# Kernel optimization log

Hardware: AMD Instinct MI355X
Metric: run time of the kernel (lower is better)

Reference implementation:

```python
import jax, jax.numpy as jnp
import numpy as np

NC = 4
X = Y = Z = 64
IMG_SHAPE = (96, 96, 96)
SPAN = 2          # FILTER_SIZE = [5,5,5]
NUM_ITER = 4
DIL = 2           # DILATION = 2.0
SMOOTH_DISTANCE_INIT = 0.3
PRIOR_DISTANCE_INIT = 0.3


def _ind(d):
    # mirrors _get_ind from the torch code
    return (d, 0) if d > 0 else (0, -d)


def _sl(a, b):
    # slice(a, -b) with -0 -> None, mirrors _negative
    return slice(a, -b if b else None)


def _offsets():
    for dx in range(-SPAN, SPAN + 1):
        for dy in range(-SPAN, SPAN + 1):
            for dz in range(-SPAN, SPAN + 1):
                yield dx, dy, dz


def _lin_resize_axis(x, axis, out):
    # 1D linear interpolation matching torch align_corners=True
    n = x.shape[axis]
    if out == n:
        return x
    pos = jnp.arange(out, dtype=x.dtype) * ((n - 1) / (out - 1))
    i0 = jnp.clip(jnp.floor(pos).astype(jnp.int32), 0, n - 1)
    i1 = jnp.clip(i0 + 1, 0, n - 1)
    w = pos - i0.astype(x.dtype)
    shp = [1] * x.ndim
    shp[axis] = out
    w = w.reshape(shp)
    return jnp.take(x, i0, axis=axis) * (1 - w) + jnp.take(x, i1, axis=axis) * w


def _resize3d(x, out_sz):
    # trilinear, align_corners=True, separable over the 3 spatial axes of [b,c,X,Y,Z]
    for ax, o in zip((2, 3, 4), out_sz):
        x = _lin_resize_axis(x, ax, o)
    return x


def _smooth_gaussian(feats):
    # feats: [b, c, X, Y, Z] -> gaussian [b, 5,5,5, X, Y, Z]
    b = feats.shape[0]
    sp = feats.shape[2:]
    g = jnp.zeros((b, 5, 5, 5) + sp, feats.dtype)
    for dx, dy, dz in _offsets():
        dx1, dx2 = _ind(dx); dy1, dy2 = _ind(dy); dz1, dz2 = _ind(dz)
        a = feats[:, :, _sl(dx1, dx2), _sl(dy1, dy2), _sl(dz1, dz2)]
        c = feats[:, :, _sl(dx2, dx1), _sl(dy2, dy1), _sl(dz2, dz1)]
        e = jnp.exp(-0.5 * jnp.sum((a - c) ** 2, axis=1))
        g = g.at[:, dx + SPAN, dy + SPAN, dz + SPAN,
                 _sl(dx2, dx1), _sl(dy2, dy1), _sl(dz2, dz1)].set(e)
    return g


def _prior_gaussian(f1, f2):
    # f1, f2: [b, c, x, y, z] (already downsampled) -> [b, 5,5,5, x, y, z]
    b = f1.shape[0]
    sp = f1.shape[2:]
    g = jnp.zeros((b, 5, 5, 5) + sp, f1.dtype)
    for dx, dy, dz in _offsets():
        dx1, dx2 = _ind(dx); dy1, dy2 = _ind(dy); dz1, dz2 = _ind(dz)
        a = f1[:, :, _sl(dx2, dx1), _sl(dy2, dy1), _sl(dz2, dz1)]
        c = f2[:, :, _sl(dx1, dx2), _sl(dy1, dy2), _sl(dz1, dz2)]
        e = jnp.exp(-0.5 * jnp.sum((a - c) ** 2, axis=1))
        g = g.at[:, dx + SPAN, dy + SPAN, dz + SPAN,
                 _sl(dx2, dx1), _sl(dy2, dy1), _sl(dz2, dz1)].set(e)
    return g


def _message(p, g):
    # p: [b, nc, x, y, z]; g: [b, 5,5,5, x, y, z]
    out = jnp.zeros_like(p)
    for dx, dy, dz in _offsets():
        dx1, dx2 = _ind(dx); dy1, dy2 = _ind(dy); dz1, dz2 = _ind(dz)
        a = p[:, :, _sl(dx1, dx2), _sl(dy1, dy2), _sl(dz1, dz2)]
        w = g[:, None, dx + SPAN, dy + SPAN, dz + SPAN,
              _sl(dx2, dx1), _sl(dy2, dy1), _sl(dz2, dz1)]
        out = out.at[:, :, _sl(dx2, dx1), _sl(dy2, dy1), _sl(dz2, dz1)].add(a * w)
    return out


def setup_inputs() -> dict:
    key = jax.random.key(0)
    ks = jax.random.split(key, 6)
    unary = jax.random.normal(ks[0], (1, NC, X, Y, Z), jnp.float32)
    img = jax.random.normal(ks[1], (1, 2, X, Y, Z), jnp.float32)
    atlas = jax.random.normal(ks[2], (1, 2, X, Y, Z), jnp.float32)
    atlas_label = jax.random.uniform(ks[3], (1, X, Y, Z, NC), jnp.float32)
    patch_start = jax.random.randint(ks[4], (1, 3), 0, 32, jnp.int32)
    return {
        "unary": unary,
        "img": img,
        "atlas": atlas,
        "atlas_label": atlas_label,
        "patch_start": patch_start,
        "smooth_norm": jnp.array([1.0 / SMOOTH_DISTANCE_INIT], jnp.float32),
        "smooth_weight": jnp.ones((NC,), jnp.float32),
        "prior_norm": jnp.array([1.0 / PRIOR_DISTANCE_INIT], jnp.float32),
        "prior_weight": jnp.ones(IMG_SHAPE, jnp.float32),
        "compat_w": jnp.eye(NC, dtype=jnp.float32),
    }


def reference(unary, img, atlas, atlas_label, patch_start,
              smooth_norm, smooth_weight, prior_norm, prior_weight, compat_w):
    b, nc, x, y, z = unary.shape
    ds = (x // DIL, y // DIL, z // DIL)  # floor(in*0.5) == ceil(in/2) for even dims

    # similarity kernels
    sg = _smooth_gaussian(img * smooth_norm)                      # [b,5,5,5,x,y,z]
    f1 = _resize3d(img * prior_norm, ds)
    f2 = _resize3d(atlas * prior_norm, ds)
    pg = _prior_gaussian(f1, f2)                                  # [b,5,5,5,x/2,y/2,z/2]

    # prior message is independent of q_values: compute once
    al = jnp.transpose(atlas_label, (0, 4, 1, 2, 3))              # [b,nc,x,y,z]
    al_ds = _resize3d(al, ds)
    pm = _resize3d(_message(al_ds, pg), (x, y, z))                # [b,nc,x,y,z]
    pw = jax.lax.dynamic_slice(
        prior_weight,
        (patch_start[0, 0], patch_start[0, 1], patch_start[0, 2]),
        (x, y, z))
    prior_term = pw[None, None] * pm

    q = unary
    for _ in range(NUM_ITER):
        p = jax.nn.softmax(q, axis=1)
        sm = _message(p, sg)
        pred = smooth_weight[None, :, None, None, None] * sm + prior_term
        q = unary + jnp.einsum('oc,bcxyz->boxyz', compat_w, pred)  # 1x1x1 compat conv
    return q
```

## Files before the change

### kernel.cpp

```cpp
#include <hip/hip_runtime.h>

#define NN 64
#define N3 (64*64*64)
#define DS 32

#define LOG2E 1.4426950408889634f
#define FSCALE 0.8493218002880191f

typedef _Float16 h2  __attribute__((ext_vector_type(2)));
typedef __fp16   h2f __attribute__((ext_vector_type(2)));

__device__ __forceinline__ float fexp2(float x) { return __builtin_amdgcn_exp2f(x); }

__device__ __forceinline__ h2 u2h(unsigned u) { union { unsigned u; h2 h; } c; c.u = u; return c.h; }
__device__ __forceinline__ unsigned h2u(h2 h) { union { unsigned u; h2 h; } c; c.h = h; return c.u; }
__device__ __forceinline__ h2 pkh(float a, float b) {
    union { h2f a; h2 b; } c; c.a = __builtin_amdgcn_cvt_pkrtz(a, b); return c.b;
}
__device__ __forceinline__ float fdot2(h2 a, h2 b) {
    union { h2 h; h2f f; } ca, cb; ca.h = a; cb.h = b;
    return __builtin_amdgcn_fdot2(ca.f, cb.f, 0.0f, false);
}


#define TXD 8
#define TYD 8
#define TZD 8
#define TZR 4
#define RZ 2
#define HX 12
#define HY 12
#define HZ 12
#define PZ 14
#define CPX 6
#define CSX 10

template<bool FIRST, bool LAST>
__global__ __launch_bounds__(1024, 8) void k_iter(
    const float* __restrict__ unary,
    const uint2* __restrict__ pin,
    const unsigned* __restrict__ fpk_in,
    const float* __restrict__ img,
    const float* __restrict__ atlas,
    const float* __restrict__ alabel,
    const float* __restrict__ pnorm,
    const float* __restrict__ snorm,
    const float* __restrict__ pweight,
    const int* __restrict__ pstart,
    const float* __restrict__ sweight,
    const float* __restrict__ compat,
    float4* __restrict__ unary4,
    unsigned* __restrict__ fpk_out,
    uint2* __restrict__ pout,
    float* __restrict__ qout)
{
    __shared__ __align__(16) unsigned char raw1[16384];
    auto nbS = reinterpret_cast<uint4 (*)[CSX][CSX]>(raw1);
    auto pS  = reinterpret_cast<uint2 (*)[HY][PZ]>(raw1);
    __shared__ __align__(8)  unsigned fS[HX][HY][PZ];
    __shared__ __align__(16) uint4    accS[3][TXD*TYD*TZR];
    __shared__ __align__(8)  uint2    pmS[CPX][CPX][CPX];

    const int tzg = threadIdx.x, ty = threadIdx.y;
    const int tx = threadIdx.z & 7, s = threadIdx.z >> 3;
    const int x0b = blockIdx.z * TXD, y0b = blockIdx.y * TYD, z0b = blockIdx.x * TZD;
    const int tid = threadIdx.x + TZR*threadIdx.y + (TZR*TYD)*threadIdx.z;

    const int tz0 = tzg * RZ;
    const int gx = x0b + tx, gy = y0b + ty;
    const int g = (gx*NN + gy)*NN + z0b + tz0;

    float4 u40, u41;
    float sw0, sw1, sw2, sw3;
    float cw[16];

    if (FIRST) {
        const int cxlo = (x0b*31)/63, cylo = (y0b*31)/63, czlo = (z0b*31)/63;
        const float pnf = pnorm[0] * FSCALE;

        if (tid < CSX*CSX*CSX) {
            int lz = tid % CSX; int r = tid / CSX; int ly = r % CSX; int lx = r / CSX;
            int cx = cxlo - 2 + lx, cy = cylo - 2 + ly, cz = czlo - 2 + lz;
            uint4 v = make_uint4(0u, 0u, 0u, 0u);
            if ((unsigned)cx < DS && (unsigned)cy < DS && (unsigned)cz < DS) {
                const float scale = 63.0f / 31.0f;
                float posx = cx*scale; int a0i = (int)posx; float wx = posx - a0i; int a1i = a0i+1 <= 63 ? a0i+1 : 63;
                float posy = cy*scale; int b0i = (int)posy; float wy = posy - b0i; int b1i = b0i+1 <= 63 ? b0i+1 : 63;
                float posz = cz*scale; int d0i = (int)posz; float wz = posz - d0i; int d1i = d0i+1 <= 63 ? d0i+1 : 63;
                float w000=(1-wx)*(1-wy)*(1-wz), w001=(1-wx)*(1-wy)*wz;
                float w010=(1-wx)*wy*(1-wz),     w011=(1-wx)*wy*wz;
                float w100=wx*(1-wy)*(1-wz),     w101=wx*(1-wy)*wz;
                float w110=wx*wy*(1-wz),         w111=wx*wy*wz;
                int c000=(a0i*NN+b0i)*NN+d0i, c001=(a0i*NN+b0i)*NN+d1i;
                int c010=(a0i*NN+b1i)*NN+d0i, c011=(a0i*NN+b1i)*NN+d1i;
                int c100=(a1i*NN+b0i)*NN+d0i, c101=(a1i*NN+b0i)*NN+d1i;
                int c110=(a1i*NN+b1i)*NN+d0i, c111=(a1i*NN+b1i)*NN+d1i;
                auto tri = [&](const float* p) -> float {
                    return p[c000]*w000 + p[c001]*w001 + p[c010]*w010 + p[c011]*w011
                         + p[c100]*w100 + p[c101]*w101 + p[c110]*w110 + p[c111]*w111;
                };
                const float4* lab = (const float4*)alabel;
                float4 l = make_float4(0.f,0.f,0.f,0.f);
                {
                    float4 t;
                    t = lab[c000]; l.x += w000*t.x; l.y += w000*t.y; l.z += w000*t.z; l.w += w000*t.w;
                    t = lab[c001]; l.x += w001*t.x; l.y += w001*t.y; l.z += w001*t.z; l.w += w001*t.w;
                    t = lab[c010]; l.x += w010*t.x; l.y += w010*t.y; l.z += w010*t.z; l.w += w010*t.w;
                    t = lab[c011]; l.x += w011*t.x; l.y += w011*t.y; l.z += w011*t.z; l.w += w011*t.w;
                    t = lab[c100]; l.x += w100*t.x; l.y += w100*t.y; l.z += w100*t.z; l.w += w100*t.w;
                    t = lab[c101]; l.x += w101*t.x; l.y += w101*t.y; l.z += w101*t.z; l.w += w101*t.w;
                    t = lab[c110]; l.x += w110*t.x; l.y += w110*t.y; l.z += w110*t.z; l.w += w110*t.w;
                    t = lab[c111]; l.x += w111*t.x; l.y += w111*t.y; l.z += w111*t.z; l.w += w111*t.w;
                }
                v = make_uint4(h2u(pkh(pnf*tri(atlas), pnf*tri(atlas + N3))),
                               h2u(pkh(l.x, l.y)), h2u(pkh(l.z, l.w)),
                               h2u(pkh(pnf*tri(img), pnf*tri(img + N3))));
            }
            nbS[lx][ly][lz] = v;
        }
        __syncthreads();

        if (tid < CPX*CPX*CPX) {
            int pz = tid % CPX; int r = tid / CPX; int py = r % CPX; int px = r / CPX;
            int cx = cxlo + px, cy = cylo + py, cz = czlo + pz;
            uint2 o = make_uint2(0u, 0u);
            if (cx < DS && cy < DS && cz < DS) {
                h2 ncf = -u2h(nbS[px+2][py+2][pz+2].w);
                float a0=0.f, a1=0.f, a2=0.f, a3=0.f;
                for (int dx = -2; dx <= 2; ++dx) {
                    int xx = cx + dx; if ((unsigned)xx >= DS) continue;
                    for (int dy = -2; dy <= 2; ++dy) {
                        int yy = cy + dy; if ((unsigned)yy >= DS) continue;
                        #pragma unroll
                        for (int dz = -2; dz <= 2; ++dz) {
                            int zz = cz + dz; if ((unsigned)zz >= DS) continue;
                            uint4 v = nbS[px+2+dx][py+2+dy][pz+2+dz];
                            h2 d = u2h(v.x) + ncf;
                            float w = fexp2(-fdot2(d, d));
                            h2 l01 = u2h(v.y), l23 = u2h(v.z);
                            a0 += w*(float)l01.x; a1 += w*(float)l01.y;
                            a2 += w*(float)l23.x; a3 += w*(float)l23.y;
                        }
                    }
                }
                o = make_uint2(h2u(pkh(a0, a1)), h2u(pkh(a2, a3)));
            }
            pmS[px][py][pz] = o;
        }
        __syncthreads();

        if (s == 0) {
            sw0 = sweight[0]; sw1 = sweight[1]; sw2 = sweight[2]; sw3 = sweight[3];
            #pragma unroll
            for (int k = 0; k < 16; ++k) cw[k] = compat[k];

            const float S13 = 31.0f / 63.0f;
            float posx = gx*S13; int xc0 = (int)posx; float wxf = posx - xc0; int xc1 = xc0 < 31 ? xc0+1 : 31;
            float posy = gy*S13; int yc0 = (int)posy; float wyf = posy - yc0; int yc1 = yc0 < 31 ? yc0+1 : 31;
            int lx0 = xc0-cxlo, lx1 = xc1-cxlo;
            int ly0 = yc0-cylo, ly1 = yc1-cylo;
            const int ps0 = pstart[0], ps1 = pstart[1], ps2 = pstart[2];

            auto up = [&](uint2 u) -> float4 {
                h2 a = u2h(u.x), b = u2h(u.y);
                return make_float4((float)a.x, (float)a.y, (float)b.x, (float)b.y);
            };

            #pragma unroll
            for (int rz = 0; rz < RZ; ++rz) {
                int gz = z0b + tz0 + rz;
                float posz = gz*S13; int zc0 = (int)posz; float wzf = posz - zc0; int zc1 = zc0 < 31 ? zc0+1 : 31;
                int lz0 = zc0-czlo, lz1 = zc1-czlo;
                float4 p000 = up(pmS[lx0][ly0][lz0]), p001 = up(pmS[lx0][ly0][lz1]);
                float4 p010 = up(pmS[lx0][ly1][lz0]), p011 = up(pmS[lx0][ly1][lz1]);
                float4 p100 = up(pmS[lx1][ly0][lz0]), p101 = up(pmS[lx1][ly0][lz1]);
                float4 p110 = up(pmS[lx1][ly1][lz0]), p111 = up(pmS[lx1][ly1][lz1]);
                float w000=(1-wxf)*(1-wyf)*(1-wzf), w001=(1-wxf)*(1-wyf)*wzf;
                float w010=(1-wxf)*wyf*(1-wzf),     w011=(1-wxf)*wyf*wzf;
                float w100=wxf*(1-wyf)*(1-wzf),     w101=wxf*(1-wyf)*wzf;
                float w110=wxf*wyf*(1-wzf),         w111=wxf*wyf*wzf;
                float pw = pweight[(ps0+gx)*96*96 + (ps1+gy)*96 + (ps2+gz)];
                float pr0 = pw*(w000*p000.x + w001*p001.x + w010*p010.x + w011*p011.x + w100*p100.x + w101*p101.x + w110*p110.x + w111*p111.x);
                float pr1 = pw*(w000*p000.y + w001*p001.y + w010*p010.y + w011*p011.y + w100*p100.y + w101*p101.y + w110*p110.y + w111*p111.y);
                float pr2 = pw*(w000*p000.z + w001*p001.z + w010*p010.z + w011*p011.z + w100*p100.z + w101*p101.z + w110*p110.z + w111*p111.z);
                float pr3 = pw*(w000*p000.w + w001*p001.w + w010*p010.w + w011*p011.w + w100*p100.w + w101*p101.w + w110*p110.w + w111*p111.w);

                int gg = g + rz;
                float4 q;
                q.x = unary[gg]      + cw[0]*pr0  + cw[1]*pr1  + cw[2]*pr2  + cw[3]*pr3;
                q.y = unary[gg+N3]   + cw[4]*pr0  + cw[5]*pr1  + cw[6]*pr2  + cw[7]*pr3;
                q.z = unary[gg+2*N3] + cw[8]*pr0  + cw[9]*pr1  + cw[10]*pr2 + cw[11]*pr3;
                q.w = unary[gg+3*N3] + cw[12]*pr0 + cw[13]*pr1 + cw[14]*pr2 + cw[15]*pr3;
                unary4[gg] = q;
                if (rz == 0) u40 = q; else u41 = q;
            }
        }
        __syncthreads();
    }

    const float sc = FIRST ? snorm[0] * FSCALE : 0.0f;
    #pragma unroll
    for (int rr = 0; rr < 2; ++rr) {
        int i = tid + rr*1024;
        if (i < HX*HY*HZ) {
            int lz = i % HZ; int r = i / HZ;
            int ly = r % HY; int lx = r / HY;
            int hgx = x0b + lx - 2, hgy = y0b + ly - 2, hgz = z0b + lz - 2;
            uint2 pu = make_uint2(0u, 0u);
            unsigned fu = 0u;
            if ((unsigned)hgx < NN && (unsigned)hgy < NN && (unsigned)hgz < NN) {
                int hg = (hgx*NN + hgy)*NN + hgz;
                if (FIRST) {
                    float q0 = unary[hg], q1 = unary[hg+N3], q2 = unary[hg+2*N3], q3 = unary[hg+3*N3];
                    float m = fmaxf(fmaxf(q0,q1), fmaxf(q2,q3));
                    float e0 = fexp2((q0-m)*LOG2E);
                    float e1 = fexp2((q1-m)*LOG2E);
                    float e2 = fexp2((q2-m)*LOG2E);
                    float e3 = fexp2((q3-m)*LOG2E);
                    float inv = 1.0f/(e0+e1+e2+e3);
                    pu = make_uint2(h2u(pkh(e0*inv, e1*inv)), h2u(pkh(e2*inv, e3*inv)));
                    fu = h2u(pkh(img[hg]*sc, img[hg+N3]*sc));
                    if ((unsigned)(lx-2) < 8u && (unsigned)(ly-2) < 8u && (unsigned)(lz-2) < 8u)
                        fpk_out[hg] = fu;
                } else {
                    pu = pin[hg];
                    fu = fpk_in[hg];
                }
            }
            pS[lx][ly][lz] = pu;
            fS[lx][ly][lz] = fu;
        }
    }

    if (!FIRST && s == 0) {
        u40 = unary4[g]; u41 = unary4[g+1];
        sw0 = sweight[0]; sw1 = sweight[1]; sw2 = sweight[2]; sw3 = sweight[3];
        #pragma unroll
        for (int k = 0; k < 16; ++k) cw[k] = compat[k];
    }

    __syncthreads();

    const h2 ncf0 = -u2h(fS[tx+2][ty+2][tz0+2]);
    const h2 ncf1 = -u2h(fS[tx+2][ty+2][tz0+3]);

    h2 a01_0 = (h2)0, a23_0 = (h2)0, a01_1 = (h2)0, a23_1 = (h2)0;

    #pragma unroll
    for (int pp = 0; pp < 7; ++pp) {
        int p = (3 - s) + 4*pp;
        if (p < 25) {
            int dx = p / 5, dy = p - 5*dx;
            const uint4* pv = reinterpret_cast<const uint4*>(&pS[tx+dx][ty+dy][tz0]);
            const uint2* fv = reinterpret_cast<const uint2*>(&fS[tx+dx][ty+dy][tz0]);
            uint4 qa = pv[0], qb = pv[1], qc = pv[2];
            uint2 fa = fv[0], fb = fv[1], fc = fv[2];

            unsigned fz[6]  = { fa.x, fa.y, fb.x, fb.y, fc.x, fc.y };
            unsigned p01[6] = { qa.x, qa.z, qb.x, qb.z, qc.x, qc.z };
            unsigned p23[6] = { qa.y, qa.w, qb.y, qb.w, qc.y, qc.w };

            #pragma unroll
            for (int dz = 0; dz < 5; ++dz) {
                {
                    h2 d = u2h(fz[dz]) + ncf0;
                    float w = fexp2(-fdot2(d, d));
                    h2 w2 = pkh(w, w);
                    a01_0 = w2 * u2h(p01[dz]) + a01_0;
                    a23_0 = w2 * u2h(p23[dz]) + a23_0;
                }
                {
                    h2 d = u2h(fz[dz+1]) + ncf1;
                    float w = fexp2(-fdot2(d, d));
                    h2 w2 = pkh(w, w);
                    a01_1 = w2 * u2h(p01[dz+1]) + a01_1;
                    a23_1 = w2 * u2h(p23[dz+1]) + a23_1;
                }
            }
        }
    }

    const int pid = (tx*TYD + ty)*TZR + tzg;
    if (s != 0) {
        accS[s-1][pid] = make_uint4(h2u(a01_0), h2u(a23_0), h2u(a01_1), h2u(a23_1));
    }
    __syncthreads();

    if (s == 0) {
        #pragma unroll
        for (int j = 0; j < 3; ++j) {
            uint4 v = accS[j][pid];
            a01_0 += u2h(v.x); a23_0 += u2h(v.y);
            a01_1 += u2h(v.z); a23_1 += u2h(v.w);
        }

        float p0, p1, p2, p3;
        float r00, r10, r20, r30, r01, r11, r21, r31;
        p0 = sw0*(float)a01_0.x; p1 = sw1*(float)a01_0.y;
        p2 = sw2*(float)a23_0.x; p3 = sw3*(float)a23_0.y;
        r00 = u40.x + cw[0]*p0  + cw[1]*p1  + cw[2]*p2  + cw[3]*p3;
        r10 = u40.y + cw[4]*p0  + cw[5]*p1  + cw[6]*p2  + cw[7]*p3;
        r20 = u40.z + cw[8]*p0  + cw[9]*p1  + cw[10]*p2 + cw[11]*p3;
        r30 = u40.w + cw[12]*p0 + cw[13]*p1 + cw[14]*p2 + cw[15]*p3;
        p0 = sw0*(float)a01_1.x; p1 = sw1*(float)a01_1.y;
        p2 = sw2*(float)a23_1.x; p3 = sw3*(float)a23_1.y;
        r01 = u41.x + cw[0]*p0  + cw[1]*p1  + cw[2]*p2  + cw[3]*p3;
        r11 = u41.y + cw[4]*p0  + cw[5]*p1  + cw[6]*p2  + cw[7]*p3;
        r21 = u41.z + cw[8]*p0  + cw[9]*p1  + cw[10]*p2 + cw[11]*p3;
        r31 = u41.w + cw[12]*p0 + cw[13]*p1 + cw[14]*p2 + cw[15]*p3;

        if (LAST) {
            *(float2*)(qout + 0*N3 + g) = make_float2(r00, r01);
            *(float2*)(qout + 1*N3 + g) = make_float2(r10, r11);
            *(float2*)(qout + 2*N3 + g) = make_float2(r20, r21);
            *(float2*)(qout + 3*N3 + g) = make_float2(r30, r31);
        } else {
            float m0 = fmaxf(fmaxf(r00,r10), fmaxf(r20,r30));
            float e00 = fexp2((r00-m0)*LOG2E), e10 = fexp2((r10-m0)*LOG2E);
            float e20 = fexp2((r20-m0)*LOG2E), e30 = fexp2((r30-m0)*LOG2E);
            float i0 = 1.0f/(e00+e10+e20+e30);
            float m1 = fmaxf(fmaxf(r01,r11), fmaxf(r21,r31));
            float e01 = fexp2((r01-m1)*LOG2E), e11 = fexp2((r11-m1)*LOG2E);
            float e21 = fexp2((r21-m1)*LOG2E), e31 = fexp2((r31-m1)*LOG2E);
            float i1 = 1.0f/(e01+e11+e21+e31);
            uint4 o = make_uint4(h2u(pkh(e00*i0, e10*i0)), h2u(pkh(e20*i0, e30*i0)),
                                 h2u(pkh(e01*i1, e11*i1)), h2u(pkh(e21*i1, e31*i1)));
            *reinterpret_cast<uint4*>(&pout[g]) = o;
        }
    }
}


extern "C" void kernel_launch(void* const* d_in, const int* in_sizes, int n_in,
                              void* d_out, int out_size, void* d_ws, size_t ws_size,
                              hipStream_t stream)
{
    const float* unary   = (const float*)d_in[0];
    const float* img     = (const float*)d_in[1];
    const float* atlas   = (const float*)d_in[2];
    const float* alabel  = (const float*)d_in[3];
    const int*   pstart  = (const int*)d_in[4];
    const float* snorm   = (const float*)d_in[5];
    const float* sweight = (const float*)d_in[6];
    const float* pnorm   = (const float*)d_in[7];
    const float* pweight = (const float*)d_in[8];
    const float* compat  = (const float*)d_in[9];
    float* out = (float*)d_out;
    float* ws  = (float*)d_ws;

    float4*   unary4 = (float4*)ws;
    uint2*    pA     = (uint2*)(ws + 4*N3);
    uint2*    pB     = (uint2*)(ws + 6*N3);
    unsigned* fpk    = (unsigned*)(ws + 8*N3);

    dim3 grid(NN/TZD, NN/TYD, NN/TXD), block(TZR, TYD, 32);
    k_iter<true, false><<<grid, block, 0, stream>>>(unary, pA, fpk, img, atlas, alabel,
        pnorm, snorm, pweight, pstart, sweight, compat, unary4, fpk, pA, out);
    k_iter<false,false><<<grid, block, 0, stream>>>(unary, pA, fpk, img, atlas, alabel,
        pnorm, snorm, pweight, pstart, sweight, compat, unary4, fpk, pB, out);
    k_iter<false,false><<<grid, block, 0, stream>>>(unary, pB, fpk, img, atlas, alabel,
        pnorm, snorm, pweight, pstart, sweight, compat, unary4, fpk, pA, out);
    k_iter<false,true ><<<grid, block, 0, stream>>>(unary, pA, fpk, img, atlas, alabel,
        pnorm, snorm, pweight, pstart, sweight, compat, unary4, fpk, pB, out);
}
```

Baseline: 90.90 us.

## Fuse pairs of mean-field iterations per launch via halo recompute

Replaces four per-iteration kernel launches with two fused launches, each running two iterations. The intermediate softmax is recomputed on a widened 12^3 halo region in shared memory, so one global round trip of the probability field and one launch boundary are removed per pair. The packed feature array is no longer written and read back from global memory; it is rebuilt from the image in each kernel. In exchange there is redundant halo computation, a larger shared-memory footprint that may cut occupancy, and more per-block work in the first stage.

```diff
diff --git a/kernel.cpp b/kernel.cpp
--- a/kernel.cpp
+++ b/kernel.cpp
@@ -23,23 +23,18 @@
 }
 
 
-#define TXD 8
-#define TYD 8
-#define TZD 8
-#define TZR 4
-#define RZ 2
-#define HX 12
-#define HY 12
-#define HZ 12
-#define PZ 14
-#define CPX 6
-#define CSX 10
-
-template<bool FIRST, bool LAST>
-__global__ __launch_bounds__(1024, 8) void k_iter(
+#define TB 8
+#define HE 16
+#define PZ2 18
+#define DE 12
+#define PZ1 14
+#define CPX 8
+#define CSX 12
+
+template<bool FIRST>
+__global__ __launch_bounds__(1024, 8) void k_fused(
     const float* __restrict__ unary,
     const uint2* __restrict__ pin,
-    const unsigned* __restrict__ fpk_in,
     const float* __restrict__ img,
     const float* __restrict__ atlas,
     const float* __restrict__ alabel,
@@ -50,78 +45,94 @@
     const float* __restrict__ sweight,
     const float* __restrict__ compat,
     float4* __restrict__ unary4,
-    unsigned* __restrict__ fpk_out,
     uint2* __restrict__ pout,
     float* __restrict__ qout)
 {
-    __shared__ __align__(16) unsigned char raw1[16384];
-    auto nbS = reinterpret_cast<uint4 (*)[CSX][CSX]>(raw1);
-    auto pS  = reinterpret_cast<uint2 (*)[HY][PZ]>(raw1);
-    __shared__ __align__(8)  unsigned fS[HX][HY][PZ];
-    __shared__ __align__(16) uint4    accS[3][TXD*TYD*TZR];
-    __shared__ __align__(8)  uint2    pmS[CPX][CPX][CPX];
-
-    const int tzg = threadIdx.x, ty = threadIdx.y;
-    const int tx = threadIdx.z & 7, s = threadIdx.z >> 3;
-    const int x0b = blockIdx.z * TXD, y0b = blockIdx.y * TYD, z0b = blockIdx.x * TZD;
-    const int tid = threadIdx.x + TZR*threadIdx.y + (TZR*TYD)*threadIdx.z;
-
-    const int tz0 = tzg * RZ;
-    const int gx = x0b + tx, gy = y0b + ty;
-    const int g = (gx*NN + gy)*NN + z0b + tz0;
-
-    float4 u40, u41;
-    float sw0, sw1, sw2, sw3;
+    __shared__ __align__(16) unsigned char region1[HE*HE*PZ2*8];
+    __shared__ __align__(16) unsigned char region2[12288];
+    __shared__ __align__(8)  unsigned fS[HE][HE][PZ2];
+
+    auto p2S  = reinterpret_cast<uint2 (*)[HE][PZ2]>(region1);
+    auto p1S  = reinterpret_cast<uint2 (*)[DE][PZ1]>(region1);
+    auto nbS  = reinterpret_cast<uint4 (*)[CSX][CSX]>(region1);
+    auto pmS  = reinterpret_cast<uint2 (*)[CPX][CPX]>(region2);
+    auto accS = reinterpret_cast<uint4 (*)[256]>(region2);
+
+    const int tid = threadIdx.x;
+    const int x0b = blockIdx.z * TB, y0b = blockIdx.y * TB, z0b = blockIdx.x * TB;
+    const float sc = snorm[0] * FSCALE;
+
+    const float sw0 = sweight[0], sw1 = sweight[1], sw2 = sweight[2], sw3 = sweight[3];
     float cw[16];
+    #pragma unroll
+    for (int k = 0; k < 16; ++k) cw[k] = compat[k];
+
+    const bool mact = tid < 864;
+    const int  mpz = tid % 6;
+    const int  mt  = tid / 6;
+    const int  mpy = mt % 12;
+    const int  mpx = mt / 12;
+    const int  mlz0 = 2 * mpz;
+    const int  mgx = x0b - 2 + mpx, mgy = y0b - 2 + mpy, mgz0 = z0b - 2 + mlz0;
+
+    float4 mu4[2];
+    mu4[0] = make_float4(0.f,0.f,0.f,0.f);
+    mu4[1] = make_float4(0.f,0.f,0.f,0.f);
 
     if (FIRST) {
-        const int cxlo = (x0b*31)/63, cylo = (y0b*31)/63, czlo = (z0b*31)/63;
+        const int cxlo = (((x0b-2 > 0) ? x0b-2 : 0) * 31) / 63;
+        const int cylo = (((y0b-2 > 0) ? y0b-2 : 0) * 31) / 63;
+        const int czlo = (((z0b-2 > 0) ? z0b-2 : 0) * 31) / 63;
         const float pnf = pnorm[0] * FSCALE;
 
-        if (tid < CSX*CSX*CSX) {
-            int lz = tid % CSX; int r = tid / CSX; int ly = r % CSX; int lx = r / CSX;
-            int cx = cxlo - 2 + lx, cy = cylo - 2 + ly, cz = czlo - 2 + lz;
-            uint4 v = make_uint4(0u, 0u, 0u, 0u);
-            if ((unsigned)cx < DS && (unsigned)cy < DS && (unsigned)cz < DS) {
-                const float scale = 63.0f / 31.0f;
-                float posx = cx*scale; int a0i = (int)posx; float wx = posx - a0i; int a1i = a0i+1 <= 63 ? a0i+1 : 63;
-                float posy = cy*scale; int b0i = (int)posy; float wy = posy - b0i; int b1i = b0i+1 <= 63 ? b0i+1 : 63;
-                float posz = cz*scale; int d0i = (int)posz; float wz = posz - d0i; int d1i = d0i+1 <= 63 ? d0i+1 : 63;
-                float w000=(1-wx)*(1-wy)*(1-wz), w001=(1-wx)*(1-wy)*wz;
-                float w010=(1-wx)*wy*(1-wz),     w011=(1-wx)*wy*wz;
-                float w100=wx*(1-wy)*(1-wz),     w101=wx*(1-wy)*wz;
-                float w110=wx*wy*(1-wz),         w111=wx*wy*wz;
-                int c000=(a0i*NN+b0i)*NN+d0i, c001=(a0i*NN+b0i)*NN+d1i;
-                int c010=(a0i*NN+b1i)*NN+d0i, c011=(a0i*NN+b1i)*NN+d1i;
-                int c100=(a1i*NN+b0i)*NN+d0i, c101=(a1i*NN+b0i)*NN+d1i;
-                int c110=(a1i*NN+b1i)*NN+d0i, c111=(a1i*NN+b1i)*NN+d1i;
-                auto tri = [&](const float* p) -> float {
-                    return p[c000]*w000 + p[c001]*w001 + p[c010]*w010 + p[c011]*w011
-                         + p[c100]*w100 + p[c101]*w101 + p[c110]*w110 + p[c111]*w111;
-                };
-                const float4* lab = (const float4*)alabel;
-                float4 l = make_float4(0.f,0.f,0.f,0.f);
-                {
-                    float4 t;
-                    t = lab[c000]; l.x += w000*t.x; l.y += w000*t.y; l.z += w000*t.z; l.w += w000*t.w;
-                    t = lab[c001]; l.x += w001*t.x; l.y += w001*t.y; l.z += w001*t.z; l.w += w001*t.w;
-                    t = lab[c010]; l.x += w010*t.x; l.y += w010*t.y; l.z += w010*t.z; l.w += w010*t.w;
-                    t = lab[c011]; l.x += w011*t.x; l.y += w011*t.y; l.z += w011*t.z; l.w += w011*t.w;
-                    t = lab[c100]; l.x += w100*t.x; l.y += w100*t.y; l.z += w100*t.z; l.w += w100*t.w;
-                    t = lab[c101]; l.x += w101*t.x; l.y += w101*t.y; l.z += w101*t.z; l.w += w101*t.w;
-                    t = lab[c110]; l.x += w110*t.x; l.y += w110*t.y; l.z += w110*t.z; l.w += w110*t.w;
-                    t = lab[c111]; l.x += w111*t.x; l.y += w111*t.y; l.z += w111*t.z; l.w += w111*t.w;
-                }
-                v = make_uint4(h2u(pkh(pnf*tri(atlas), pnf*tri(atlas + N3))),
-                               h2u(pkh(l.x, l.y)), h2u(pkh(l.z, l.w)),
-                               h2u(pkh(pnf*tri(img), pnf*tri(img + N3))));
-            }
-            nbS[lx][ly][lz] = v;
+        #pragma unroll
+        for (int r = 0; r < 2; ++r) {
+            int i = tid + r*1024;
+            if (i < CSX*CSX*CSX) {
+                int lz = i % CSX; int t = i / CSX; int ly = t % CSX; int lx = t / CSX;
+                int cx = cxlo - 2 + lx, cy = cylo - 2 + ly, cz = czlo - 2 + lz;
+                uint4 v = make_uint4(0u, 0u, 0u, 0u);
+                if ((unsigned)cx < DS && (unsigned)cy < DS && (unsigned)cz < DS) {
+                    const float scale = 63.0f / 31.0f;
+                    float posx = cx*scale; int a0i = (int)posx; float wx = posx - a0i; int a1i = a0i+1 <= 63 ? a0i+1 : 63;
+                    float posy = cy*scale; int b0i = (int)posy; float wy = posy - b0i; int b1i = b0i+1 <= 63 ? b0i+1 : 63;
+                    float posz = cz*scale; int d0i = (int)posz; float wz = posz - d0i; int d1i = d0i+1 <= 63 ? d0i+1 : 63;
+                    float w000=(1-wx)*(1-wy)*(1-wz), w001=(1-wx)*(1-wy)*wz;
+                    float w010=(1-wx)*wy*(1-wz),     w011=(1-wx)*wy*wz;
+                    float w100=wx*(1-wy)*(1-wz),     w101=wx*(1-wy)*wz;
+                    float w110=wx*wy*(1-wz),         w111=wx*wy*wz;
+                    int c000=(a0i*NN+b0i)*NN+d0i, c001=(a0i*NN+b0i)*NN+d1i;
+                    int c010=(a0i*NN+b1i)*NN+d0i, c011=(a0i*NN+b1i)*NN+d1i;
+                    int c100=(a1i*NN+b0i)*NN+d0i, c101=(a1i*NN+b0i)*NN+d1i;
+                    int c110=(a1i*NN+b1i)*NN+d0i, c111=(a1i*NN+b1i)*NN+d1i;
+                    auto tri = [&](const float* p) -> float {
+                        return p[c000]*w000 + p[c001]*w001 + p[c010]*w010 + p[c011]*w011
+                             + p[c100]*w100 + p[c101]*w101 + p[c110]*w110 + p[c111]*w111;
+                    };
+                    const float4* lab = (const float4*)alabel;
+                    float4 l = make_float4(0.f,0.f,0.f,0.f);
+                    {
+                        float4 t4;
+                        t4 = lab[c000]; l.x += w000*t4.x; l.y += w000*t4.y; l.z += w000*t4.z; l.w += w000*t4.w;
+                        t4 = lab[c001]; l.x += w001*t4.x; l.y += w001*t4.y; l.z += w001*t4.z; l.w += w001*t4.w;
+                        t4 = lab[c010]; l.x += w010*t4.x; l.y += w010*t4.y; l.z += w010*t4.z; l.w += w010*t4.w;
+                        t4 = lab[c011]; l.x += w011*t4.x; l.y += w011*t4.y; l.z += w011*t4.z; l.w += w011*t4.w;
+                        t4 = lab[c100]; l.x += w100*t4.x; l.y += w100*t4.y; l.z += w100*t4.z; l.w += w100*t4.w;
+                        t4 = lab[c101]; l.x += w101*t4.x; l.y += w101*t4.y; l.z += w101*t4.z; l.w += w101*t4.w;
+                        t4 = lab[c110]; l.x += w110*t4.x; l.y += w110*t4.y; l.z += w110*t4.z; l.w += w110*t4.w;
+                        t4 = lab[c111]; l.x += w111*t4.x; l.y += w111*t4.y; l.z += w111*t4.z; l.w += w111*t4.w;
+                    }
+                    v = make_uint4(h2u(pkh(pnf*tri(atlas), pnf*tri(atlas + N3))),
+                                   h2u(pkh(l.x, l.y)), h2u(pkh(l.z, l.w)),
+                                   h2u(pkh(pnf*tri(img), pnf*tri(img + N3))));
+                }
+                nbS[lx][ly][lz] = v;
+            }
         }
         __syncthreads();
 
         if (tid < CPX*CPX*CPX) {
-            int pz = tid % CPX; int r = tid / CPX; int py = r % CPX; int px = r / CPX;
+            int pz = tid & 7; int py = (tid >> 3) & 7; int px = tid >> 6;
             int cx = cxlo + px, cy = cylo + py, cz = czlo + pz;
             uint2 o = make_uint2(0u, 0u);
             if (cx < DS && cy < DS && cz < DS) {
@@ -149,100 +160,171 @@
         }
         __syncthreads();
 
-        if (s == 0) {
-            sw0 = sweight[0]; sw1 = sweight[1]; sw2 = sweight[2]; sw3 = sweight[3];
-            #pragma unroll
-            for (int k = 0; k < 16; ++k) cw[k] = compat[k];
-
+        if (mact) {
             const float S13 = 31.0f / 63.0f;
-            float posx = gx*S13; int xc0 = (int)posx; float wxf = posx - xc0; int xc1 = xc0 < 31 ? xc0+1 : 31;
-            float posy = gy*S13; int yc0 = (int)posy; float wyf = posy - yc0; int yc1 = yc0 < 31 ? yc0+1 : 31;
-            int lx0 = xc0-cxlo, lx1 = xc1-cxlo;
-            int ly0 = yc0-cylo, ly1 = yc1-cylo;
             const int ps0 = pstart[0], ps1 = pstart[1], ps2 = pstart[2];
-
-            auto up = [&](uint2 u) -> float4 {
-                h2 a = u2h(u.x), b = u2h(u.y);
-                return make_float4((float)a.x, (float)a.y, (float)b.x, (float)b.y);
-            };
-
-            #pragma unroll
-            for (int rz = 0; rz < RZ; ++rz) {
-                int gz = z0b + tz0 + rz;
-                float posz = gz*S13; int zc0 = (int)posz; float wzf = posz - zc0; int zc1 = zc0 < 31 ? zc0+1 : 31;
-                int lz0 = zc0-czlo, lz1 = zc1-czlo;
-                float4 p000 = up(pmS[lx0][ly0][lz0]), p001 = up(pmS[lx0][ly0][lz1]);
-                float4 p010 = up(pmS[lx0][ly1][lz0]), p011 = up(pmS[lx0][ly1][lz1]);
-                float4 p100 = up(pmS[lx1][ly0][lz0]), p101 = up(pmS[lx1][ly0][lz1]);
-                float4 p110 = up(pmS[lx1][ly1][lz0]), p111 = up(pmS[lx1][ly1][lz1]);
-                float w000=(1-wxf)*(1-wyf)*(1-wzf), w001=(1-wxf)*(1-wyf)*wzf;
-                float w010=(1-wxf)*wyf*(1-wzf),     w011=(1-wxf)*wyf*wzf;
-                float w100=wxf*(1-wyf)*(1-wzf),     w101=wxf*(1-wyf)*wzf;
-                float w110=wxf*wyf*(1-wzf),         w111=wxf*wyf*wzf;
-                float pw = pweight[(ps0+gx)*96*96 + (ps1+gy)*96 + (ps2+gz)];
-                float pr0 = pw*(w000*p000.x + w001*p001.x + w010*p010.x + w011*p011.x + w100*p100.x + w101*p101.x + w110*p110.x + w111*p111.x);
-                float pr1 = pw*(w000*p000.y + w001*p001.y + w010*p010.y + w011*p011.y + w100*p100.y + w101*p101.y + w110*p110.y + w111*p111.y);
-                float pr2 = pw*(w000*p000.z + w001*p001.z + w010*p010.z + w011*p011.z + w100*p100.z + w101*p101.z + w110*p110.z + w111*p111.z);
-                float pr3 = pw*(w000*p000.w + w001*p001.w + w010*p010.w + w011*p011.w + w100*p100.w + w101*p101.w + w110*p110.w + w111*p111.w);
-
-                int gg = g + rz;
-                float4 q;
-                q.x = unary[gg]      + cw[0]*pr0  + cw[1]*pr1  + cw[2]*pr2  + cw[3]*pr3;
-                q.y = unary[gg+N3]   + cw[4]*pr0  + cw[5]*pr1  + cw[6]*pr2  + cw[7]*pr3;
-                q.z = unary[gg+2*N3] + cw[8]*pr0  + cw[9]*pr1  + cw[10]*pr2 + cw[11]*pr3;
-                q.w = unary[gg+3*N3] + cw[12]*pr0 + cw[13]*pr1 + cw[14]*pr2 + cw[15]*pr3;
-                unary4[gg] = q;
-                if (rz == 0) u40 = q; else u41 = q;
-            }
-        }
-        __syncthreads();
-    }
-
-    const float sc = FIRST ? snorm[0] * FSCALE : 0.0f;
+            if ((unsigned)mgx < NN && (unsigned)mgy < NN) {
+                float posx = mgx*S13; int xc0 = (int)posx; float wxf = posx - xc0; int xc1 = xc0 < 31 ? xc0+1 : 31;
+                float posy = mgy*S13; int yc0 = (int)posy; float wyf = posy - yc0; int yc1 = yc0 < 31 ? yc0+1 : 31;
+                int lx0 = xc0-cxlo, lx1 = xc1-cxlo;
+                int ly0 = yc0-cylo, ly1 = yc1-cylo;
+                auto up = [&](uint2 u) -> float4 {
+                    h2 a = u2h(u.x), b = u2h(u.y);
+                    return make_float4((float)a.x, (float)a.y, (float)b.x, (float)b.y);
+                };
+                #pragma unroll
+                for (int rz = 0; rz < 2; ++rz) {
+                    int gz = mgz0 + rz;
+                    if ((unsigned)gz >= NN) continue;
+                    float posz = gz*S13; int zc0 = (int)posz; float wzf = posz - zc0; int zc1 = zc0 < 31 ? zc0+1 : 31;
+                    int lz0c = zc0-czlo, lz1c = zc1-czlo;
+                    float4 p000 = up(pmS[lx0][ly0][lz0c]), p001 = up(pmS[lx0][ly0][lz1c]);
+                    float4 p010 = up(pmS[lx0][ly1][lz0c]), p011 = up(pmS[lx0][ly1][lz1c]);
+                    float4 p100 = up(pmS[lx1][ly0][lz0c]), p101 = up(pmS[lx1][ly0][lz1c]);
+                    float4 p110 = up(pmS[lx1][ly1][lz0c]), p111 = up(pmS[lx1][ly1][lz1c]);
+                    float w000=(1-wxf)*(1-wyf)*(1-wzf), w001=(1-wxf)*(1-wyf)*wzf;
+                    float w010=(1-wxf)*wyf*(1-wzf),     w011=(1-wxf)*wyf*wzf;
+                    float w100=wxf*(1-wyf)*(1-wzf),     w101=wxf*(1-wyf)*wzf;
+                    float w110=wxf*wyf*(1-wzf),         w111=wxf*wyf*wzf;
+                    float pw = pweight[(ps0+mgx)*96*96 + (ps1+mgy)*96 + (ps2+gz)];
+                    float pr0 = pw*(w000*p000.x + w001*p001.x + w010*p010.x + w011*p011.x + w100*p100.x + w101*p101.x + w110*p110.x + w111*p111.x);
+                    float pr1 = pw*(w000*p000.y + w001*p001.y + w010*p010.y + w011*p011.y + w100*p100.y + w101*p101.y + w110*p110.y + w111*p111.y);
+                    float pr2 = pw*(w000*p000.z + w001*p001.z + w010*p010.z + w011*p011.z + w100*p100.z + w101*p101.z + w110*p110.z + w111*p111.z);
+                    float pr3 = pw*(w000*p000.w + w001*p001.w + w010*p010.w + w011*p011.w + w100*p100.w + w101*p101.w + w110*p110.w + w111*p111.w);
+                    int gg = (mgx*NN + mgy)*NN + gz;
+                    float4 q;
+                    q.x = unary[gg]      + cw[0]*pr0  + cw[1]*pr1  + cw[2]*pr2  + cw[3]*pr3;
+                    q.y = unary[gg+N3]   + cw[4]*pr0  + cw[5]*pr1  + cw[6]*pr2  + cw[7]*pr3;
+                    q.z = unary[gg+2*N3] + cw[8]*pr0  + cw[9]*pr1  + cw[10]*pr2 + cw[11]*pr3;
+                    q.w = unary[gg+3*N3] + cw[12]*pr0 + cw[13]*pr1 + cw[14]*pr2 + cw[15]*pr3;
+                    mu4[rz] = q;
+                    if ((unsigned)(mpx-2) < 8u && (unsigned)(mpy-2) < 8u && (unsigned)(mlz0+rz-2) < 8u)
+                        unary4[gg] = q;
+                }
+            }
+        }
+    }
+
     #pragma unroll
-    for (int rr = 0; rr < 2; ++rr) {
-        int i = tid + rr*1024;
-        if (i < HX*HY*HZ) {
-            int lz = i % HZ; int r = i / HZ;
-            int ly = r % HY; int lx = r / HY;
-            int hgx = x0b + lx - 2, hgy = y0b + ly - 2, hgz = z0b + lz - 2;
-            uint2 pu = make_uint2(0u, 0u);
-            unsigned fu = 0u;
-            if ((unsigned)hgx < NN && (unsigned)hgy < NN && (unsigned)hgz < NN) {
-                int hg = (hgx*NN + hgy)*NN + hgz;
-                if (FIRST) {
-                    float q0 = unary[hg], q1 = unary[hg+N3], q2 = unary[hg+2*N3], q3 = unary[hg+3*N3];
-                    float m = fmaxf(fmaxf(q0,q1), fmaxf(q2,q3));
-                    float e0 = fexp2((q0-m)*LOG2E);
-                    float e1 = fexp2((q1-m)*LOG2E);
-                    float e2 = fexp2((q2-m)*LOG2E);
-                    float e3 = fexp2((q3-m)*LOG2E);
-                    float inv = 1.0f/(e0+e1+e2+e3);
-                    pu = make_uint2(h2u(pkh(e0*inv, e1*inv)), h2u(pkh(e2*inv, e3*inv)));
-                    fu = h2u(pkh(img[hg]*sc, img[hg+N3]*sc));
-                    if ((unsigned)(lx-2) < 8u && (unsigned)(ly-2) < 8u && (unsigned)(lz-2) < 8u)
-                        fpk_out[hg] = fu;
-                } else {
-                    pu = pin[hg];
-                    fu = fpk_in[hg];
-                }
-            }
-            pS[lx][ly][lz] = pu;
-            fS[lx][ly][lz] = fu;
-        }
-    }
-
-    if (!FIRST && s == 0) {
-        u40 = unary4[g]; u41 = unary4[g+1];
-        sw0 = sweight[0]; sw1 = sweight[1]; sw2 = sweight[2]; sw3 = sweight[3];
-        #pragma unroll
-        for (int k = 0; k < 16; ++k) cw[k] = compat[k];
-    }
-
+    for (int r = 0; r < 4; ++r) {
+        int i = tid + r*1024;
+        int lz = i & 15, ly = (i >> 4) & 15, lx = i >> 8;
+        int gx = x0b + lx - 4, gy = y0b + ly - 4, gz = z0b + lz - 4;
+        uint2 pu = make_uint2(0u, 0u);
+        unsigned fu = 0u;
+        if ((unsigned)gx < NN && (unsigned)gy < NN && (unsigned)gz < NN) {
+            int g = (gx*NN + gy)*NN + gz;
+            if (FIRST) {
+                float q0 = unary[g], q1 = unary[g+N3], q2 = unary[g+2*N3], q3 = unary[g+3*N3];
+                float m = fmaxf(fmaxf(q0,q1), fmaxf(q2,q3));
+                float e0 = fexp2((q0-m)*LOG2E);
+                float e1 = fexp2((q1-m)*LOG2E);
+                float e2 = fexp2((q2-m)*LOG2E);
+                float e3 = fexp2((q3-m)*LOG2E);
+                float inv = 1.0f/(e0+e1+e2+e3);
+                pu = make_uint2(h2u(pkh(e0*inv, e1*inv)), h2u(pkh(e2*inv, e3*inv)));
+            } else {
+                pu = pin[g];
+            }
+            fu = h2u(pkh(img[g]*sc, img[g+N3]*sc));
+        }
+        p2S[lx][ly][lz] = pu;
+        fS[lx][ly][lz] = fu;
+    }
+
+    if (!FIRST && mact) {
+        if ((unsigned)mgx < NN && (unsigned)mgy < NN) {
+            if ((unsigned)mgz0 < NN)       mu4[0] = unary4[(mgx*NN + mgy)*NN + mgz0];
+            if ((unsigned)(mgz0+1) < NN)   mu4[1] = unary4[(mgx*NN + mgy)*NN + mgz0 + 1];
+        }
+    }
     __syncthreads();
 
-    const h2 ncf0 = -u2h(fS[tx+2][ty+2][tz0+2]);
-    const h2 ncf1 = -u2h(fS[tx+2][ty+2][tz0+3]);
+    uint2 p1r0 = make_uint2(0u,0u), p1r1 = make_uint2(0u,0u);
+    if (mact) {
+        const h2 ncf0 = -u2h(fS[mpx+2][mpy+2][mlz0+2]);
+        const h2 ncf1 = -u2h(fS[mpx+2][mpy+2][mlz0+3]);
+        h2 a01_0 = (h2)0, a23_0 = (h2)0, a01_1 = (h2)0, a23_1 = (h2)0;
+
+        for (int dx = 0; dx < 5; ++dx) {
+            for (int dy = 0; dy < 5; ++dy) {
+                const uint4* pv = reinterpret_cast<const uint4*>(&p2S[mpx+dx][mpy+dy][mlz0]);
+                const uint2* fv = reinterpret_cast<const uint2*>(&fS[mpx+dx][mpy+dy][mlz0]);
+                uint4 qa = pv[0], qb = pv[1], qc = pv[2];
+                uint2 fa = fv[0], fb = fv[1], fc = fv[2];
+                unsigned fz[6]  = { fa.x, fa.y, fb.x, fb.y, fc.x, fc.y };
+                unsigned p01[6] = { qa.x, qa.z, qb.x, qb.z, qc.x, qc.z };
+                unsigned p23[6] = { qa.y, qa.w, qb.y, qb.w, qc.y, qc.w };
+                #pragma unroll
+                for (int dz = 0; dz < 5; ++dz) {
+                    {
+                        h2 d = u2h(fz[dz]) + ncf0;
+                        float w = fexp2(-fdot2(d, d));
+                        h2 w2 = pkh(w, w);
+                        a01_0 = w2 * u2h(p01[dz]) + a01_0;
+                        a23_0 = w2 * u2h(p23[dz]) + a23_0;
+                    }
+                    {
+                        h2 d = u2h(fz[dz+1]) + ncf1;
+                        float w = fexp2(-fdot2(d, d));
+                        h2 w2 = pkh(w, w);
+                        a01_1 = w2 * u2h(p01[dz+1]) + a01_1;
+                        a23_1 = w2 * u2h(p23[dz+1]) + a23_1;
+                    }
+                }
+            }
+        }
+
+        if ((unsigned)mgx < NN && (unsigned)mgy < NN) {
+            if ((unsigned)mgz0 < NN) {
+                float m0 = sw0*(float)a01_0.x, m1 = sw1*(float)a01_0.y;
+                float m2 = sw2*(float)a23_0.x, m3 = sw3*(float)a23_0.y;
+                float q0 = mu4[0].x + cw[0]*m0  + cw[1]*m1  + cw[2]*m2  + cw[3]*m3;
+                float q1 = mu4[0].y + cw[4]*m0  + cw[5]*m1  + cw[6]*m2  + cw[7]*m3;
+                float q2 = mu4[0].z + cw[8]*m0  + cw[9]*m1  + cw[10]*m2 + cw[11]*m3;
+                float q3 = mu4[0].w + cw[12]*m0 + cw[13]*m1 + cw[14]*m2 + cw[15]*m3;
+                float mm = fmaxf(fmaxf(q0,q1), fmaxf(q2,q3));
+                float e0 = fexp2((q0-mm)*LOG2E), e1 = fexp2((q1-mm)*LOG2E);
+                float e2 = fexp2((q2-mm)*LOG2E), e3 = fexp2((q3-mm)*LOG2E);
+                float inv = 1.0f/(e0+e1+e2+e3);
+                p1r0 = make_uint2(h2u(pkh(e0*inv, e1*inv)), h2u(pkh(e2*inv, e3*inv)));
+            }
+            if ((unsigned)(mgz0+1) < NN) {
+                float m0 = sw0*(float)a01_1.x, m1 = sw1*(float)a01_1.y;
+                float m2 = sw2*(float)a23_1.x, m3 = sw3*(float)a23_1.y;
+                float q0 = mu4[1].x + cw[0]*m0  + cw[1]*m1  + cw[2]*m2  + cw[3]*m3;
+                float q1 = mu4[1].y + cw[4]*m0  + cw[5]*m1  + cw[6]*m2  + cw[7]*m3;
+                float q2 = mu4[1].z + cw[8]*m0  + cw[9]*m1  + cw[10]*m2 + cw[11]*m3;
+                float q3 = mu4[1].w + cw[12]*m0 + cw[13]*m1 + cw[14]*m2 + cw[15]*m3;
+                float mm = fmaxf(fmaxf(q0,q1), fmaxf(q2,q3));
+                float e0 = fexp2((q0-mm)*LOG2E), e1 = fexp2((q1-mm)*LOG2E);
+                float e2 = fexp2((q2-mm)*LOG2E), e3 = fexp2((q3-mm)*LOG2E);
+                float inv = 1.0f/(e0+e1+e2+e3);
+                p1r1 = make_uint2(h2u(pkh(e0*inv, e1*inv)), h2u(pkh(e2*inv, e3*inv)));
+            }
+        }
+    }
+    __syncthreads();
+
+    if (mact) {
+        *reinterpret_cast<uint4*>(&p1S[mpx][mpy][mlz0]) =
+            make_uint4(p1r0.x, p1r0.y, p1r1.x, p1r1.y);
+    }
+    __syncthreads();
+
+    const int tzg = tid & 3;
+    const int ty  = (tid >> 2) & 7;
+    const int tx  = (tid >> 5) & 7;
+    const int s   = tid >> 8;
+    const int tz0 = tzg * 2;
+    const int gx = x0b + tx, gy = y0b + ty;
+    const int g = (gx*NN + gy)*NN + z0b + tz0;
+
+    float4 u40, u41;
+    if (s == 0) { u40 = unary4[g]; u41 = unary4[g+1]; }
+
+    const h2 ncf0 = -u2h(fS[tx+4][ty+4][tz0+4]);
+    const h2 ncf1 = -u2h(fS[tx+4][ty+4][tz0+5]);
 
     h2 a01_0 = (h2)0, a23_0 = (h2)0, a01_1 = (h2)0, a23_1 = (h2)0;
 
@@ -251,15 +333,13 @@
         int p = (3 - s) + 4*pp;
         if (p < 25) {
             int dx = p / 5, dy = p - 5*dx;
-            const uint4* pv = reinterpret_cast<const uint4*>(&pS[tx+dx][ty+dy][tz0]);
-            const uint2* fv = reinterpret_cast<const uint2*>(&fS[tx+dx][ty+dy][tz0]);
+            const uint4* pv = reinterpret_cast<const uint4*>(&p1S[tx+dx][ty+dy][tz0]);
+            const uint2* fv = reinterpret_cast<const uint2*>(&fS[tx+dx+2][ty+dy+2][tz0+2]);
             uint4 qa = pv[0], qb = pv[1], qc = pv[2];
             uint2 fa = fv[0], fb = fv[1], fc = fv[2];
-
             unsigned fz[6]  = { fa.x, fa.y, fb.x, fb.y, fc.x, fc.y };
             unsigned p01[6] = { qa.x, qa.z, qb.x, qb.z, qc.x, qc.z };
             unsigned p23[6] = { qa.y, qa.w, qb.y, qb.w, qc.y, qc.w };
-
             #pragma unroll
             for (int dz = 0; dz < 5; ++dz) {
                 {
@@ -280,7 +360,7 @@
         }
     }
 
-    const int pid = (tx*TYD + ty)*TZR + tzg;
+    const int pid = (tx*8 + ty)*4 + tzg;
     if (s != 0) {
         accS[s-1][pid] = make_uint4(h2u(a01_0), h2u(a23_0), h2u(a01_1), h2u(a23_1));
     }
@@ -294,38 +374,38 @@
             a01_1 += u2h(v.z); a23_1 += u2h(v.w);
         }
 
-        float p0, p1, p2, p3;
+        float m0, m1, m2, m3;
         float r00, r10, r20, r30, r01, r11, r21, r31;
-        p0 = sw0*(float)a01_0.x; p1 = sw1*(float)a01_0.y;
-        p2 = sw2*(float)a23_0.x; p3 = sw3*(float)a23_0.y;
-        r00 = u40.x + cw[0]*p0  + cw[1]*p1  + cw[2]*p2  + cw[3]*p3;
-        r10 = u40.y + cw[4]*p0  + cw[5]*p1  + cw[6]*p2  + cw[7]*p3;
-        r20 = u40.z + cw[8]*p0  + cw[9]*p1  + cw[10]*p2 + cw[11]*p3;
-        r30 = u40.w + cw[12]*p0 + cw[13]*p1 + cw[14]*p2 + cw[15]*p3;
-        p0 = sw0*(float)a01_1.x; p1 = sw1*(float)a01_1.y;
-        p2 = sw2*(float)a23_1.x; p3 = sw3*(float)a23_1.y;
-        r01 = u41.x + cw[0]*p0  + cw[1]*p1  + cw[2]*p2  + cw[3]*p3;
-        r11 = u41.y + cw[4]*p0  + cw[5]*p1  + cw[6]*p2  + cw[7]*p3;
-        r21 = u41.z + cw[8]*p0  + cw[9]*p1  + cw[10]*p2 + cw[11]*p3;
-        r31 = u41.w + cw[12]*p0 + cw[13]*p1 + cw[14]*p2 + cw[15]*p3;
-
-        if (LAST) {
+        m0 = sw0*(float)a01_0.x; m1 = sw1*(float)a01_0.y;
+        m2 = sw2*(float)a23_0.x; m3 = sw3*(float)a23_0.y;
+        r00 = u40.x + cw[0]*m0  + cw[1]*m1  + cw[2]*m2  + cw[3]*m3;
+        r10 = u40.y + cw[4]*m0  + cw[5]*m1  + cw[6]*m2  + cw[7]*m3;
+        r20 = u40.z + cw[8]*m0  + cw[9]*m1  + cw[10]*m2 + cw[11]*m3;
+        r30 = u40.w + cw[12]*m0 + cw[13]*m1 + cw[14]*m2 + cw[15]*m3;
+        m0 = sw0*(float)a01_1.x; m1 = sw1*(float)a01_1.y;
+        m2 = sw2*(float)a23_1.x; m3 = sw3*(float)a23_1.y;
+        r01 = u41.x + cw[0]*m0  + cw[1]*m1  + cw[2]*m2  + cw[3]*m3;
+        r11 = u41.y + cw[4]*m0  + cw[5]*m1  + cw[6]*m2  + cw[7]*m3;
+        r21 = u41.z + cw[8]*m0  + cw[9]*m1  + cw[10]*m2 + cw[11]*m3;
+        r31 = u41.w + cw[12]*m0 + cw[13]*m1 + cw[14]*m2 + cw[15]*m3;
+
+        if (FIRST) {
+            float mm0 = fmaxf(fmaxf(r00,r10), fmaxf(r20,r30));
+            float e00 = fexp2((r00-mm0)*LOG2E), e10 = fexp2((r10-mm0)*LOG2E);
+            float e20 = fexp2((r20-mm0)*LOG2E), e30 = fexp2((r30-mm0)*LOG2E);
+            float i0 = 1.0f/(e00+e10+e20+e30);
+            float mm1 = fmaxf(fmaxf(r01,r11), fmaxf(r21,r31));
+            float e01 = fexp2((r01-mm1)*LOG2E), e11 = fexp2((r11-mm1)*LOG2E);
+            float e21 = fexp2((r21-mm1)*LOG2E), e31 = fexp2((r31-mm1)*LOG2E);
+            float i1 = 1.0f/(e01+e11+e21+e31);
+            uint4 o = make_uint4(h2u(pkh(e00*i0, e10*i0)), h2u(pkh(e20*i0, e30*i0)),
+                                 h2u(pkh(e01*i1, e11*i1)), h2u(pkh(e21*i1, e31*i1)));
+            *reinterpret_cast<uint4*>(&pout[g]) = o;
+        } else {
             *(float2*)(qout + 0*N3 + g) = make_float2(r00, r01);
             *(float2*)(qout + 1*N3 + g) = make_float2(r10, r11);
             *(float2*)(qout + 2*N3 + g) = make_float2(r20, r21);
             *(float2*)(qout + 3*N3 + g) = make_float2(r30, r31);
-        } else {
-            float m0 = fmaxf(fmaxf(r00,r10), fmaxf(r20,r30));
-            float e00 = fexp2((r00-m0)*LOG2E), e10 = fexp2((r10-m0)*LOG2E);
-            float e20 = fexp2((r20-m0)*LOG2E), e30 = fexp2((r30-m0)*LOG2E);
-            float i0 = 1.0f/(e00+e10+e20+e30);
-            float m1 = fmaxf(fmaxf(r01,r11), fmaxf(r21,r31));
-            float e01 = fexp2((r01-m1)*LOG2E), e11 = fexp2((r11-m1)*LOG2E);
-            float e21 = fexp2((r21-m1)*LOG2E), e31 = fexp2((r31-m1)*LOG2E);
-            float i1 = 1.0f/(e01+e11+e21+e31);
-            uint4 o = make_uint4(h2u(pkh(e00*i0, e10*i0)), h2u(pkh(e20*i0, e30*i0)),
-                                 h2u(pkh(e01*i1, e11*i1)), h2u(pkh(e21*i1, e31*i1)));
-            *reinterpret_cast<uint4*>(&pout[g]) = o;
         }
     }
 }
@@ -348,18 +428,14 @@
     float* out = (float*)d_out;
     float* ws  = (float*)d_ws;
 
-    float4*   unary4 = (float4*)ws;
-    uint2*    pA     = (uint2*)(ws + 4*N3);
-    uint2*    pB     = (uint2*)(ws + 6*N3);
-    unsigned* fpk    = (unsigned*)(ws + 8*N3);
-
-    dim3 grid(NN/TZD, NN/TYD, NN/TXD), block(TZR, TYD, 32);
-    k_iter<true, false><<<grid, block, 0, stream>>>(unary, pA, fpk, img, atlas, alabel,
-        pnorm, snorm, pweight, pstart, sweight, compat, unary4, fpk, pA, out);
-    k_iter<false,false><<<grid, block, 0, stream>>>(unary, pA, fpk, img, atlas, alabel,
-        pnorm, snorm, pweight, pstart, sweight, compat, unary4, fpk, pB, out);
-    k_iter<false,false><<<grid, block, 0, stream>>>(unary, pB, fpk, img, atlas, alabel,
-        pnorm, snorm, pweight, pstart, sweight, compat, unary4, fpk, pA, out);
-    k_iter<false,true ><<<grid, block, 0, stream>>>(unary, pA, fpk, img, atlas, alabel,
-        pnorm, snorm, pweight, pstart, sweight, compat, unary4, fpk, pB, out);
+    float4* unary4 = (float4*)ws;
+    uint2*  pA     = (uint2*)(ws + 4*N3);
+
+    dim3 grid(NN/TB, NN/TB, NN/TB), block(1024);
+    k_fused<true ><<<grid, block, 0, stream>>>(unary, pA, img, atlas, alabel, pnorm, snorm,
+                                               pweight, pstart, sweight, compat,
+                                               unary4, pA, out);
+    k_fused<false><<<grid, block, 0, stream>>>(unary, pA, img, atlas, alabel, pnorm, snorm,
+                                               pweight, pstart, sweight, compat,
+                                               unary4, pA, out);
 }
```

Measured after the change: 142.6 us. 56.8% more time.
